# Kernel tuning notes

Measured on AMD Instinct MI355X. Metric: run time of the kernel, lower is better.

The kernel has to match this reference:

```python
import jax, jax.numpy as jnp
import numpy as np

# B videos, K topological sorts, N subtask nodes, S video segments, H = hsize
B, K, N, S, H = 8, 4, 16, 64, 512
NEG = -100.0  # torch.full((N,S), -100.0) init in dp_align


def setup_inputs() -> dict:
    key = jax.random.key(0)
    ks = jax.random.split(key, 6)
    return {
        "seg_text_feats": jax.random.normal(ks[0], (B, K, N, 2 * H), jnp.float32),
        "vid_feature": jax.random.normal(ks[1], (B, S, 2 * H), jnp.float32),
        "labels": jax.random.uniform(ks[2], (B,), jnp.float32),
        "W1": jax.random.normal(ks[3], (4 * H, H), jnp.float32) * 0.02,
        "b1": jnp.zeros((H,), jnp.float32),
        "w2": jax.random.normal(ks[4], (H,), jnp.float32) * 0.04,
        "b2": jnp.zeros((), jnp.float32),
    }


def _dp_single(logits):
    """Viterbi-style banded DP of dp_align for one (video, sort) pair.
    logits: [N, S]. Returns (best_score=arr[0,0], aggregated_logits, alignment[N]).
    Recurrence (faithful to the torch code):
      arr[n,s] = max(V_curr, arr[n,s+1]) where
        V_curr = logsig(logit[n,s])                     if n == N-1
        V_curr = logsig(logit[n,s]) + arr[n+1, s]       otherwise
      band: s in [n, S-N+n]; out-of-band cells stay -100.
    """
    n_nodes, n_segs = logits.shape
    L = jax.nn.log_sigmoid(logits)
    s_idx = jnp.arange(n_segs)

    def row_step(arr_next, xn):
        n, Ln = xn
        c = jnp.where(n == n_nodes - 1, Ln, Ln + arr_next)  # V_opt_curr per segment
        in_band = (s_idx >= n) & (s_idx <= n_segs - n_nodes + n)
        # arr[n,s] = max(max_{s'>=s in band} c[s'], -100)  (reverse cummax == seg loop)
        cm = jax.lax.cummax(jnp.where(in_band, c, -jnp.inf)[::-1])[::-1]
        row = jnp.where(in_band, jnp.maximum(cm, NEG), NEG)
        # choice[s]: took V_opt_curr (ties -> curr, matching >=); base case s=S-1 forced curr
        row_nxt = jnp.concatenate([row[1:], jnp.full((1,), -1e30, row.dtype)])
        choice = in_band & (c >= row_nxt)
        return row, (row, choice)

    arr0 = jnp.full((n_segs,), NEG, logits.dtype)
    xs = (jnp.arange(n_nodes - 1, -1, -1), L[::-1])  # nodes processed bottom-up
    _, (rows, choices) = jax.lax.scan(row_step, arr0, xs)
    best = rows[-1][0]          # arr[0, 0]
    choice = choices[::-1]      # reorder to ascending node index

    # Backpointer traceback: curr -> (node+1, seg+1) (record seg), next -> (node, seg+1)
    def step(state, _):
        node, seg, done, agg, align = state
        took = (~done) & choice[node, seg]
        agg = agg + jnp.where(took, logits[node, seg], 0.0)
        align = align.at[node].set(jnp.where(took, seg, align[node]))
        done = done | (took & (node == n_nodes - 1))
        node = jnp.where(took & (~done), node + 1, node)
        seg = jnp.where(done, seg, jnp.minimum(seg + 1, n_segs - 1))
        return (node, seg, done, agg, align), None

    init = (jnp.int32(0), jnp.int32(0), jnp.bool_(False),
            jnp.zeros((), logits.dtype), jnp.zeros((n_nodes,), jnp.int32))
    (_, _, _, agg, align), _ = jax.lax.scan(step, init, None, length=n_nodes + n_segs)
    return best, agg, align


def reference(seg_text_feats, vid_feature, labels, W1, b1, w2, b2):
    Bx, Kx, Nx, F2 = seg_text_feats.shape
    Sx = vid_feature.shape[1]
    # Batched query MLP over all (sort, node, segment) pairs (replaces the per-pair
    # batch-1 Linear+ReLU+Linear launches in the torch loop). Dropout(0.5) is eval-mode identity.
    t = jnp.broadcast_to(seg_text_feats[:, :, :, None, :], (Bx, Kx, Nx, Sx, F2))
    v = jnp.broadcast_to(vid_feature[:, None, None, :, :], (Bx, Kx, Nx, Sx, F2))
    cat = jnp.concatenate([t, v], axis=-1)                      # [B,K,N,S,4H]
    h1 = jax.nn.relu(jnp.einsum('bknsf,fh->bknsh', cat, W1) + b1)
    logits = jnp.einsum('bknsh,h->bkns', h1, w2) + b2           # [B,K,N,S]

    best, agg, align = jax.vmap(jax.vmap(_dp_single))(logits)   # [B,K], [B,K], [B,K,N]
    k = jnp.argmax(best, axis=-1)                               # best sort per video
    agg_b = jnp.take_along_axis(agg, k[:, None], axis=1)[:, 0]
    align_b = jnp.take_along_axis(align, k[:, None, None], axis=1)[:, 0]
    probs = jax.nn.sigmoid(agg_b)                               # ent_probs, [B]
    return probs, labels, align_b
```

## Files before the change

### kernel.cpp

```cpp
#include <hip/hip_runtime.h>
#include <math.h>

#define Bsz 8
#define Kc 4
#define Nn 16
#define Ss 64
#define Hh 512
#define F2 1024

__device__ __forceinline__ float logsigf(float x) {
    return fminf(x, 0.0f) - log1pf(expf(-fabsf(x)));
}

__global__ __launch_bounds__(256) void gemm_kernel(
    const float* __restrict__ seg, const float* __restrict__ vid,
    const float* __restrict__ W1, float* __restrict__ outbuf, int nsplit)
{
    const int z = blockIdx.z / nsplit;
    const int q = blockIdx.z % nsplit;
    const int Kq = F2 / nsplit;
    const int kbase = q * Kq;
    const float* __restrict__ Amat = z ? vid : seg;
    const float* __restrict__ Bmat = W1 + (z ? (size_t)F2 * Hh : 0);
    float* __restrict__ Out = outbuf + (size_t)blockIdx.z * (512 * Hh);
    const int r0 = blockIdx.x * 64;
    const int n0 = blockIdx.y * 64;
    __shared__ __align__(16) float As[2][32][68];
    __shared__ __align__(16) float Bs[2][32][64];
    const int t = threadIdx.x;
    const int mt = (t >> 4) << 2;
    const int nt = (t & 15) << 2;
    const int a_row = t >> 3;
    const int a_k4  = (t & 7) << 2;
    const int b_kk  = t >> 4;
    const int b_c4  = (t & 15) << 2;

    float4 ra0, ra1, rb0, rb1;
    auto load_step = [&](int s) {
        const int k0 = kbase + s * 32;
        ra0 = *reinterpret_cast<const float4*>(Amat + (size_t)(r0 + a_row) * F2 + k0 + a_k4);
        ra1 = *reinterpret_cast<const float4*>(Amat + (size_t)(r0 + a_row + 32) * F2 + k0 + a_k4);
        rb0 = *reinterpret_cast<const float4*>(Bmat + (size_t)(k0 + b_kk) * Hh + n0 + b_c4);
        rb1 = *reinterpret_cast<const float4*>(Bmat + (size_t)(k0 + b_kk + 16) * Hh + n0 + b_c4);
    };
    auto write_step = [&](int buf) {
        As[buf][a_k4 + 0][a_row] = ra0.x; As[buf][a_k4 + 1][a_row] = ra0.y;
        As[buf][a_k4 + 2][a_row] = ra0.z; As[buf][a_k4 + 3][a_row] = ra0.w;
        As[buf][a_k4 + 0][a_row + 32] = ra1.x; As[buf][a_k4 + 1][a_row + 32] = ra1.y;
        As[buf][a_k4 + 2][a_row + 32] = ra1.z; As[buf][a_k4 + 3][a_row + 32] = ra1.w;
        *reinterpret_cast<float4*>(&Bs[buf][b_kk][b_c4]) = rb0;
        *reinterpret_cast<float4*>(&Bs[buf][b_kk + 16][b_c4]) = rb1;
    };

    float acc[4][4] = {{0.f}};
    load_step(0);
    write_step(0);
    __syncthreads();
    const int steps = Kq / 32;
    for (int s = 0; s < steps; ++s) {
        const int cur = s & 1;
        if (s + 1 < steps) load_step(s + 1);
        #pragma unroll
        for (int kk = 0; kk < 32; ++kk) {
            float4 a4 = *reinterpret_cast<const float4*>(&As[cur][kk][mt]);
            float4 b4 = *reinterpret_cast<const float4*>(&Bs[cur][kk][nt]);
            float av[4] = {a4.x, a4.y, a4.z, a4.w};
            float bv[4] = {b4.x, b4.y, b4.z, b4.w};
            #pragma unroll
            for (int i2 = 0; i2 < 4; ++i2)
                #pragma unroll
                for (int j2 = 0; j2 < 4; ++j2)
                    acc[i2][j2] = fmaf(av[i2], bv[j2], acc[i2][j2]);
        }
        if (s + 1 < steps) {
            write_step(cur ^ 1);
            __syncthreads();
        }
    }
    #pragma unroll
    for (int i = 0; i < 4; ++i) {
        float4 o = make_float4(acc[i][0], acc[i][1], acc[i][2], acc[i][3]);
        *reinterpret_cast<float4*>(Out + (size_t)(r0 + mt + i) * Hh + n0 + nt) = o;
    }
}

__global__ __launch_bounds__(256) void reduce_kernel(
    const float* __restrict__ Tbuf, const float* __restrict__ b1,
    float* __restrict__ Tfin, float* __restrict__ Vfin, int nsplit)
{
    const int idx = blockIdx.x * 256 + threadIdx.x;
    const int half = idx >> 16;
    const int off4 = idx & 65535;
    const float4* src = reinterpret_cast<const float4*>(Tbuf)
                      + (size_t)half * nsplit * 65536 + off4;
    float4 a = src[0];
    for (int p = 1; p < nsplit; ++p) {
        float4 v = src[(size_t)p * 65536];
        a.x += v.x; a.y += v.y; a.z += v.z; a.w += v.w;
    }
    if (half == 0) {
        const int h = (off4 & 127) << 2;
        a.x += b1[h]; a.y += b1[h + 1]; a.z += b1[h + 2]; a.w += b1[h + 3];
        reinterpret_cast<float4*>(Tfin)[off4] = a;
    } else {
        reinterpret_cast<float4*>(Vfin)[off4] = a;
    }
}

__global__ __launch_bounds__(256) void combine_kernel(
    const float* __restrict__ Tfin, const float* __restrict__ Vfin,
    const float* __restrict__ w2, const float* __restrict__ b2,
    float* __restrict__ logits)
{
    const int bid = blockIdx.x;
    const int b  = bid >> 5;
    const int sc = (bid >> 2) & 7;
    const int rq = bid & 3;
    const int t = threadIdx.x;
    const int wave = t >> 6, lane = t & 63;
    __shared__ float Vs[8][520];
    {
        const int s_l = t & 7;
        const int h0  = (t >> 3) << 4;
        const float* row = Vfin + (size_t)(b * Ss + sc * 8 + s_l) * Hh + h0;
        #pragma unroll
        for (int x4 = 0; x4 < 4; ++x4)
            *reinterpret_cast<float4*>(&Vs[s_l][h0 + 4 * x4]) =
                *reinterpret_cast<const float4*>(row + 4 * x4);
    }
    float w2r[8];
    #pragma unroll
    for (int j = 0; j < 8; ++j) w2r[j] = w2[lane + 64 * j];
    const float bias2 = b2[0];
    __syncthreads();
    #pragma unroll
    for (int i = 0; i < 4; ++i) {
        const int kn = rq * 16 + wave * 4 + i;
        const int r  = b * 64 + kn;
        const float* trow = Tfin + (size_t)r * Hh;
        float tj[8];
        #pragma unroll
        for (int j = 0; j < 8; ++j) tj[j] = trow[lane + 64 * j];
        #pragma unroll
        for (int s = 0; s < 8; ++s) {
            float sum = 0.f;
            #pragma unroll
            for (int j = 0; j < 8; ++j)
                sum = fmaf(fmaxf(tj[j] + Vs[s][lane + 64 * j], 0.f), w2r[j], sum);
            #pragma unroll
            for (int off = 32; off > 0; off >>= 1) sum += __shfl_xor(sum, off);
            if (lane == 0) logits[(size_t)r * Ss + sc * 8 + s] = sum + bias2;
        }
    }
}

__global__ __launch_bounds__(256) void dp_kernel(
    const float* __restrict__ logits, const float* __restrict__ labels,
    float* __restrict__ out)
{
    const int b = blockIdx.x;
    const int t = threadIdx.x;
    const int k = t >> 6, lane = t & 63;
    const float* lg = logits + (size_t)((b * Kc + k) * Nn) * Ss;
    float lv[Nn], L[Nn];
    #pragma unroll
    for (int n = 0; n < Nn; ++n) {
        lv[n] = lg[n * Ss + lane];
        L[n] = logsigf(lv[n]);
    }
    float arr = -100.0f;
    unsigned long long msk[Nn];
    #pragma unroll
    for (int n = Nn - 1; n >= 0; --n) {
        float c = (n == Nn - 1) ? L[n] : (L[n] + arr);
        bool in_band = (lane >= n) && (lane <= (Ss - Nn) + n);
        float m = in_band ? c : -INFINITY;
        #pragma unroll
        for (int off = 1; off < 64; off <<= 1) {
            float o = __shfl(m, min(lane + off, 63));
            m = fmaxf(m, o);
        }
        float row = in_band ? fmaxf(m, -100.0f) : -100.0f;
        float rn = __shfl(row, min(lane + 1, 63));
        if (lane == 63) rn = -1e30f;
        msk[n] = __ballot(in_band && (c >= rn));
        arr = row;
    }
    const float best = __shfl(arr, 0);
    float agg = 0.f;
    int start = 0;
    int alignv[Nn];
    bool dead = false;
    #pragma unroll
    for (int n = 0; n < Nn; ++n) {
        unsigned long long m2 = dead ? 0ull : (msk[n] & (~0ull << start));
        if (m2) {
            const int s = __builtin_ctzll(m2);
            agg += __shfl(lv[n], s);
            alignv[n] = s;
            start = s + 1;
        } else {
            alignv[n] = 0;
            dead = true;
        }
    }
    __shared__ float bestS[Kc], aggS[Kc];
    __shared__ int alS[Kc][Nn];
    if (lane == 0) {
        bestS[k] = best; aggS[k] = agg;
        #pragma unroll
        for (int n = 0; n < Nn; ++n) alS[k][n] = alignv[n];
    }
    __syncthreads();
    if (t == 0) {
        int kb = 0; float bb = bestS[0];
        #pragma unroll
        for (int kk = 1; kk < Kc; ++kk)
            if (bestS[kk] > bb) { bb = bestS[kk]; kb = kk; }
        out[b] = 1.0f / (1.0f + expf(-aggS[kb]));
        out[Bsz + b] = labels[b];
        #pragma unroll
        for (int n = 0; n < Nn; ++n)
            out[2 * Bsz + b * Nn + n] = (float)alS[kb][n];
    }
}

extern "C" void kernel_launch(void* const* d_in, const int* in_sizes, int n_in,
                              void* d_out, int out_size, void* d_ws, size_t ws_size,
                              hipStream_t stream) {
    const float* seg    = (const float*)d_in[0];
    const float* vid    = (const float*)d_in[1];
    const float* labels = (const float*)d_in[2];
    const float* W1     = (const float*)d_in[3];
    const float* b1     = (const float*)d_in[4];
    const float* w2     = (const float*)d_in[5];
    const float* b2     = (const float*)d_in[6];
    float* out = (float*)d_out;

    const size_t part = (size_t)512 * Hh;
    int nsplit = 8;
    while (nsplit > 1 &&
           ((size_t)(2 * nsplit) * part + 2 * part + 32768) * sizeof(float) > ws_size)
        nsplit >>= 1;

    float* Tbuf   = (float*)d_ws;
    float* Tfin   = Tbuf + (size_t)(2 * nsplit) * part;
    float* Vfin   = Tfin + part;
    float* logits = Vfin + part;

    dim3 g1(8, 8, 2 * nsplit);
    hipLaunchKernelGGL(gemm_kernel, g1, dim3(256), 0, stream, seg, vid, W1, Tbuf, nsplit);
    hipLaunchKernelGGL(reduce_kernel, dim3(512), dim3(256), 0, stream,
                       Tbuf, b1, Tfin, Vfin, nsplit);
    hipLaunchKernelGGL(combine_kernel, dim3(256), dim3(256), 0, stream,
                       Tfin, Vfin, w2, b2, logits);
    hipLaunchKernelGGL(dp_kernel, dim3(Bsz), dim3(256), 0, stream, logits, labels, out);
}
```

Measured before the change: 59.42 us.

## Drop split-K reduce kernel and fuse DP into combine via last-block counter

The GEMM no longer splits K across eight grid slices written to a scratch buffer. Each 512-thread block now splits K between two 256-thread halves and reduces them through shared memory, writing Tfin/Vfin directly, so the separate reduce kernel goes away. The b1 bias is folded into the combine stage. The DP is fused into the combine kernel: an atomic ticket counter per video lets the last of its 32 blocks run the Viterbi DP, cutting four launches to two. The trade-off is fewer GEMM blocks (256 vs 1024) with longer K loops, plus reliance on threadfence and atomics and on the GEMM kernel resetting the tick counters.

```diff
diff --git a/kernel.cpp b/kernel.cpp
--- a/kernel.cpp
+++ b/kernel.cpp
@@ -12,105 +12,99 @@
     return fminf(x, 0.0f) - log1pf(expf(-fabsf(x)));
 }
 
-__global__ __launch_bounds__(256) void gemm_kernel(
+__global__ __launch_bounds__(512) void gemm_kernel(
     const float* __restrict__ seg, const float* __restrict__ vid,
-    const float* __restrict__ W1, float* __restrict__ outbuf, int nsplit)
+    const float* __restrict__ W1,
+    float* __restrict__ Tfin, float* __restrict__ Vfin, int* __restrict__ tick)
 {
-    const int z = blockIdx.z / nsplit;
-    const int q = blockIdx.z % nsplit;
-    const int Kq = F2 / nsplit;
-    const int kbase = q * Kq;
+    const int z = blockIdx.z;
     const float* __restrict__ Amat = z ? vid : seg;
     const float* __restrict__ Bmat = W1 + (z ? (size_t)F2 * Hh : 0);
-    float* __restrict__ Out = outbuf + (size_t)blockIdx.z * (512 * Hh);
+    float* __restrict__ Out = z ? Vfin : Tfin;
     const int r0 = blockIdx.x * 64;
-    const int n0 = blockIdx.y * 64;
-    __shared__ __align__(16) float As[2][32][68];
-    __shared__ __align__(16) float Bs[2][32][64];
+    const int n0 = blockIdx.y * 32;
     const int t = threadIdx.x;
-    const int mt = (t >> 4) << 2;
-    const int nt = (t & 15) << 2;
-    const int a_row = t >> 3;
-    const int a_k4  = (t & 7) << 2;
-    const int b_kk  = t >> 4;
-    const int b_c4  = (t & 15) << 2;
-
-    float4 ra0, ra1, rb0, rb1;
+
+    if (blockIdx.x == 0 && blockIdx.y == 0 && z == 0 && t < Bsz) tick[t] = 0;
+
+    const int h   = t >> 8;
+    const int tid = t & 255;
+
+    __shared__ __align__(16) float As[2][2][32][68];
+    __shared__ __align__(16) float Bs[2][2][32][36];
+
+    const int mt = (tid >> 4) << 2;
+    const int nt = (tid & 15) << 1;
+    const int ar  = tid >> 3;
+    const int ak4 = (tid & 7) << 2;
+    const int bk  = tid >> 3;
+    const int bc4 = (tid & 7) << 2;
+
+    float4 ra0, ra1, rb0;
     auto load_step = [&](int s) {
-        const int k0 = kbase + s * 32;
-        ra0 = *reinterpret_cast<const float4*>(Amat + (size_t)(r0 + a_row) * F2 + k0 + a_k4);
-        ra1 = *reinterpret_cast<const float4*>(Amat + (size_t)(r0 + a_row + 32) * F2 + k0 + a_k4);
-        rb0 = *reinterpret_cast<const float4*>(Bmat + (size_t)(k0 + b_kk) * Hh + n0 + b_c4);
-        rb1 = *reinterpret_cast<const float4*>(Bmat + (size_t)(k0 + b_kk + 16) * Hh + n0 + b_c4);
+        const int k0 = h * 512 + s * 32;
+        ra0 = *reinterpret_cast<const float4*>(Amat + (size_t)(r0 + ar) * F2 + k0 + ak4);
+        ra1 = *reinterpret_cast<const float4*>(Amat + (size_t)(r0 + ar + 32) * F2 + k0 + ak4);
+        rb0 = *reinterpret_cast<const float4*>(Bmat + (size_t)(k0 + bk) * Hh + n0 + bc4);
     };
     auto write_step = [&](int buf) {
-        As[buf][a_k4 + 0][a_row] = ra0.x; As[buf][a_k4 + 1][a_row] = ra0.y;
-        As[buf][a_k4 + 2][a_row] = ra0.z; As[buf][a_k4 + 3][a_row] = ra0.w;
-        As[buf][a_k4 + 0][a_row + 32] = ra1.x; As[buf][a_k4 + 1][a_row + 32] = ra1.y;
-        As[buf][a_k4 + 2][a_row + 32] = ra1.z; As[buf][a_k4 + 3][a_row + 32] = ra1.w;
-        *reinterpret_cast<float4*>(&Bs[buf][b_kk][b_c4]) = rb0;
-        *reinterpret_cast<float4*>(&Bs[buf][b_kk + 16][b_c4]) = rb1;
+        As[h][buf][ak4 + 0][ar] = ra0.x; As[h][buf][ak4 + 1][ar] = ra0.y;
+        As[h][buf][ak4 + 2][ar] = ra0.z; As[h][buf][ak4 + 3][ar] = ra0.w;
+        As[h][buf][ak4 + 0][ar + 32] = ra1.x; As[h][buf][ak4 + 1][ar + 32] = ra1.y;
+        As[h][buf][ak4 + 2][ar + 32] = ra1.z; As[h][buf][ak4 + 3][ar + 32] = ra1.w;
+        *reinterpret_cast<float4*>(&Bs[h][buf][bk][bc4]) = rb0;
     };
 
-    float acc[4][4] = {{0.f}};
+    float acc[4][2] = {{0.f}};
     load_step(0);
     write_step(0);
     __syncthreads();
-    const int steps = Kq / 32;
-    for (int s = 0; s < steps; ++s) {
+    #pragma unroll 1
+    for (int s = 0; s < 16; ++s) {
         const int cur = s & 1;
-        if (s + 1 < steps) load_step(s + 1);
+        if (s + 1 < 16) load_step(s + 1);
         #pragma unroll
         for (int kk = 0; kk < 32; ++kk) {
-            float4 a4 = *reinterpret_cast<const float4*>(&As[cur][kk][mt]);
-            float4 b4 = *reinterpret_cast<const float4*>(&Bs[cur][kk][nt]);
+            float4 a4 = *reinterpret_cast<const float4*>(&As[h][cur][kk][mt]);
+            float2 b2 = *reinterpret_cast<const float2*>(&Bs[h][cur][kk][nt]);
             float av[4] = {a4.x, a4.y, a4.z, a4.w};
-            float bv[4] = {b4.x, b4.y, b4.z, b4.w};
             #pragma unroll
-            for (int i2 = 0; i2 < 4; ++i2)
-                #pragma unroll
-                for (int j2 = 0; j2 < 4; ++j2)
-                    acc[i2][j2] = fmaf(av[i2], bv[j2], acc[i2][j2]);
-        }
-        if (s + 1 < steps) {
+            for (int i = 0; i < 4; ++i) {
+                acc[i][0] = fmaf(av[i], b2.x, acc[i][0]);
+                acc[i][1] = fmaf(av[i], b2.y, acc[i][1]);
+            }
+        }
+        if (s + 1 < 16) {
             write_step(cur ^ 1);
             __syncthreads();
         }
     }
-    #pragma unroll
-    for (int i = 0; i < 4; ++i) {
-        float4 o = make_float4(acc[i][0], acc[i][1], acc[i][2], acc[i][3]);
-        *reinterpret_cast<float4*>(Out + (size_t)(r0 + mt + i) * Hh + n0 + nt) = o;
-    }
-}
-
-__global__ __launch_bounds__(256) void reduce_kernel(
-    const float* __restrict__ Tbuf, const float* __restrict__ b1,
-    float* __restrict__ Tfin, float* __restrict__ Vfin, int nsplit)
-{
-    const int idx = blockIdx.x * 256 + threadIdx.x;
-    const int half = idx >> 16;
-    const int off4 = idx & 65535;
-    const float4* src = reinterpret_cast<const float4*>(Tbuf)
-                      + (size_t)half * nsplit * 65536 + off4;
-    float4 a = src[0];
-    for (int p = 1; p < nsplit; ++p) {
-        float4 v = src[(size_t)p * 65536];
-        a.x += v.x; a.y += v.y; a.z += v.z; a.w += v.w;
-    }
-    if (half == 0) {
-        const int h = (off4 & 127) << 2;
-        a.x += b1[h]; a.y += b1[h + 1]; a.z += b1[h + 2]; a.w += b1[h + 3];
-        reinterpret_cast<float4*>(Tfin)[off4] = a;
-    } else {
-        reinterpret_cast<float4*>(Vfin)[off4] = a;
-    }
-}
-
-__global__ __launch_bounds__(256) void combine_kernel(
+    __syncthreads();
+    float* red = &As[0][0][0][0];
+    if (h == 1) {
+        #pragma unroll
+        for (int i = 0; i < 4; ++i) {
+            red[tid * 8 + i * 2 + 0] = acc[i][0];
+            red[tid * 8 + i * 2 + 1] = acc[i][1];
+        }
+    }
+    __syncthreads();
+    if (h == 0) {
+        #pragma unroll
+        for (int i = 0; i < 4; ++i) {
+            float2 o;
+            o.x = acc[i][0] + red[tid * 8 + i * 2 + 0];
+            o.y = acc[i][1] + red[tid * 8 + i * 2 + 1];
+            *reinterpret_cast<float2*>(Out + (size_t)(r0 + mt + i) * Hh + n0 + nt) = o;
+        }
+    }
+}
+
+__global__ __launch_bounds__(256) void combine_dp_kernel(
     const float* __restrict__ Tfin, const float* __restrict__ Vfin,
-    const float* __restrict__ w2, const float* __restrict__ b2,
-    float* __restrict__ logits)
+    const float* __restrict__ b1, const float* __restrict__ w2,
+    const float* __restrict__ b2, const float* __restrict__ labels,
+    float* __restrict__ logits, int* __restrict__ tick, float* __restrict__ out)
 {
     const int bid = blockIdx.x;
     const int b  = bid >> 5;
@@ -119,6 +113,7 @@
     const int t = threadIdx.x;
     const int wave = t >> 6, lane = t & 63;
     __shared__ float Vs[8][520];
+    __shared__ int lastFlag;
     {
         const int s_l = t & 7;
         const int h0  = (t >> 3) << 4;
@@ -128,9 +123,9 @@
             *reinterpret_cast<float4*>(&Vs[s_l][h0 + 4 * x4]) =
                 *reinterpret_cast<const float4*>(row + 4 * x4);
     }
-    float w2r[8];
-    #pragma unroll
-    for (int j = 0; j < 8; ++j) w2r[j] = w2[lane + 64 * j];
+    float w2r[8], b1r[8];
+    #pragma unroll
+    for (int j = 0; j < 8; ++j) { w2r[j] = w2[lane + 64 * j]; b1r[j] = b1[lane + 64 * j]; }
     const float bias2 = b2[0];
     __syncthreads();
     #pragma unroll
@@ -140,7 +135,7 @@
         const float* trow = Tfin + (size_t)r * Hh;
         float tj[8];
         #pragma unroll
-        for (int j = 0; j < 8; ++j) tj[j] = trow[lane + 64 * j];
+        for (int j = 0; j < 8; ++j) tj[j] = trow[lane + 64 * j] + b1r[j];
         #pragma unroll
         for (int s = 0; s < 8; ++s) {
             float sum = 0.f;
@@ -152,15 +147,14 @@
             if (lane == 0) logits[(size_t)r * Ss + sc * 8 + s] = sum + bias2;
         }
     }
-}
-
-__global__ __launch_bounds__(256) void dp_kernel(
-    const float* __restrict__ logits, const float* __restrict__ labels,
-    float* __restrict__ out)
-{
-    const int b = blockIdx.x;
-    const int t = threadIdx.x;
-    const int k = t >> 6, lane = t & 63;
+    __threadfence();
+    __syncthreads();
+    if (t == 0) lastFlag = (atomicAdd(&tick[b], 1) == 31) ? 1 : 0;
+    __syncthreads();
+    if (!lastFlag) return;
+    __threadfence();
+
+    const int k = wave;
     const float* lg = logits + (size_t)((b * Kc + k) * Nn) * Ss;
     float lv[Nn], L[Nn];
     #pragma unroll
@@ -204,6 +198,7 @@
             dead = true;
         }
     }
+    __syncthreads();
     __shared__ float bestS[Kc], aggS[Kc];
     __shared__ int alS[Kc][Nn];
     if (lane == 0) {
@@ -237,22 +232,13 @@
     const float* b2     = (const float*)d_in[6];
     float* out = (float*)d_out;
 
-    const size_t part = (size_t)512 * Hh;
-    int nsplit = 8;
-    while (nsplit > 1 &&
-           ((size_t)(2 * nsplit) * part + 2 * part + 32768) * sizeof(float) > ws_size)
-        nsplit >>= 1;
-
-    float* Tbuf   = (float*)d_ws;
-    float* Tfin   = Tbuf + (size_t)(2 * nsplit) * part;
-    float* Vfin   = Tfin + part;
-    float* logits = Vfin + part;
-
-    dim3 g1(8, 8, 2 * nsplit);
-    hipLaunchKernelGGL(gemm_kernel, g1, dim3(256), 0, stream, seg, vid, W1, Tbuf, nsplit);
-    hipLaunchKernelGGL(reduce_kernel, dim3(512), dim3(256), 0, stream,
-                       Tbuf, b1, Tfin, Vfin, nsplit);
-    hipLaunchKernelGGL(combine_kernel, dim3(256), dim3(256), 0, stream,
-                       Tfin, Vfin, w2, b2, logits);
-    hipLaunchKernelGGL(dp_kernel, dim3(Bsz), dim3(256), 0, stream, logits, labels, out);
-}
+    float* Tfin   = (float*)d_ws;
+    float* Vfin   = Tfin + (size_t)512 * Hh;
+    float* logits = Vfin + (size_t)512 * Hh;
+    int*   tick   = (int*)(logits + 32768);
+
+    hipLaunchKernelGGL(gemm_kernel, dim3(8, 16, 2), dim3(512), 0, stream,
+                       seg, vid, W1, Tfin, Vfin, tick);
+    hipLaunchKernelGGL(combine_dp_kernel, dim3(256), dim3(256), 0, stream,
+                       Tfin, Vfin, b1, w2, b2, labels, logits, tick, out);
+}
```

After: 73.89 us. 24.4% more time.
